# Kernel optimization log

Measured on AMD Instinct MI355X. Metric: run time of the kernel, lower is better.

## Reference

```python
import jax, jax.numpy as jnp
import numpy as np

HID = 128
N_NODES = 50000
N_EDGES = 640000
N_GRAPHS = 64
N_LAYERS = 3
LN_EPS = 1e-5


def _ln(h, g, b):
    mu = jnp.mean(h, axis=-1, keepdims=True)
    v = jnp.mean(jnp.square(h - mu), axis=-1, keepdims=True)
    return (h - mu) * jax.lax.rsqrt(v + LN_EPS) * g + b


def _mlp2(h, W1, b1, g, be, W2, b2):
    # Linear -> ReLU -> LayerNorm -> (Dropout=identity in eval) -> Linear
    h = _ln(jax.nn.relu(h @ W1.T + b1), g, be)
    return h @ W2.T + b2


def _forward(x, edge_index, batch, axis_W1, axis_b1, axis_g, axis_be, axis_W2, axis_b2, org_W1, org_b1, org_g, org_be, org_W2, org_b2, nin_W, nin_b, conv_W1, conv_b1, conv_g, conv_be, conv_W2, conv_b2, eps, ln_g, ln_b, gate_W1, gate_b1, gate_g, gate_be, gate_W2, gate_b2, head_W1, head_b1, head_g, head_be, head_W2, head_b2):
    axis = x[:, 9:12]
    origin = x[:, 12:15]
    others = jnp.concatenate([x[:, :9], x[:, 15:19]], axis=1)  # [N, 13]
    axis_z = _mlp2(axis, axis_W1, axis_b1, axis_g, axis_be, axis_W2, axis_b2)
    org_z = _mlp2(origin, org_W1, org_b1, org_g, org_be, org_W2, org_b2)
    h = jnp.concatenate([others, axis_z, org_z], axis=1) @ nin_W.T + nin_b  # [N, HID]
    src, dst = edge_index[0], edge_index[1]
    n = x.shape[0]
    for l in range(N_LAYERS):
        res = h
        # GIN: sum-aggregate source features into targets (gather + scatter-add)
        agg = jax.ops.segment_sum(h[src], dst, num_segments=n)
        m = (1.0 + eps[l]) * h + agg
        m = _mlp2(m, conv_W1[l], conv_b1[l], conv_g[l], conv_be[l], conv_W2[l], conv_b2[l])
        h = _ln(jax.nn.relu(m), ln_g[l], ln_b[l]) + res
    # AttentionalAggregation: segment softmax over per-graph node gates
    gate = _mlp2(h, gate_W1, gate_b1, gate_g, gate_be, gate_W2, gate_b2)  # [N, 1]
    gmax = jax.ops.segment_max(gate, batch, num_segments=N_GRAPHS)
    e = jnp.exp(gate - gmax[batch])
    denom = jax.ops.segment_sum(e, batch, num_segments=N_GRAPHS)
    attn = e / denom[batch]
    g = jax.ops.segment_sum(attn * h, batch, num_segments=N_GRAPHS)  # [B, HID]
    logit = _mlp2(g, head_W1, head_b1, head_g, head_be, head_W2, head_b2)[:, 0]
    return logit


def setup_inputs() -> dict:
    key = jax.random.key(0)
    ks = iter(jax.random.split(key, 64))
    nk = lambda: next(ks)
    lin = lambda o, i: jax.random.normal(nk(), (o, i), jnp.float32) / np.float32(np.sqrt(i))
    lin3 = lambda L, o, i: jnp.stack([lin(o, i) for _ in range(L)])
    z = lambda *s: jnp.zeros(s, jnp.float32)
    o = lambda *s: jnp.ones(s, jnp.float32)
    inp = {}
    inp['x'] = jax.random.normal(nk(), (N_NODES, 19), jnp.float32)
    inp['edge_index'] = jax.random.randint(nk(), (2, N_EDGES), 0, N_NODES)
    inp['batch'] = jnp.sort(jax.random.randint(nk(), (N_NODES,), 0, N_GRAPHS))
    for p in ('axis', 'org'):
        inp[p + '_W1'] = lin(16, 3); inp[p + '_b1'] = z(16)
        inp[p + '_g'] = o(16); inp[p + '_be'] = z(16)
        inp[p + '_W2'] = lin(16, 16); inp[p + '_b2'] = z(16)
    inp['nin_W'] = lin(HID, 45); inp['nin_b'] = z(HID)
    inp['conv_W1'] = lin3(N_LAYERS, HID, HID); inp['conv_b1'] = z(N_LAYERS, HID)
    inp['conv_g'] = o(N_LAYERS, HID); inp['conv_be'] = z(N_LAYERS, HID)
    inp['conv_W2'] = lin3(N_LAYERS, HID, HID); inp['conv_b2'] = z(N_LAYERS, HID)
    inp['eps'] = z(N_LAYERS)
    inp['ln_g'] = o(N_LAYERS, HID); inp['ln_b'] = z(N_LAYERS, HID)
    for p in ('gate', 'head'):
        inp[p + '_W1'] = lin(HID // 2, HID); inp[p + '_b1'] = z(HID // 2)
        inp[p + '_g'] = o(HID // 2); inp[p + '_be'] = z(HID // 2)
        inp[p + '_W2'] = lin(1, HID // 2); inp[p + '_b2'] = z(1)
    return inp


def reference(x, edge_index, batch, axis_W1, axis_b1, axis_g, axis_be, axis_W2, axis_b2, org_W1, org_b1, org_g, org_be, org_W2, org_b2, nin_W, nin_b, conv_W1, conv_b1, conv_g, conv_be, conv_W2, conv_b2, eps, ln_g, ln_b, gate_W1, gate_b1, gate_g, gate_be, gate_W2, gate_b2, head_W1, head_b1, head_g, head_be, head_W2, head_b2):
    return _forward(x, edge_index, batch, axis_W1, axis_b1, axis_g, axis_be, axis_W2, axis_b2, org_W1, org_b1, org_g, org_be, org_W2, org_b2, nin_W, nin_b, conv_W1, conv_b1, conv_g, conv_be, conv_W2, conv_b2, eps, ln_g, ln_b, gate_W1, gate_b1, gate_g, gate_be, gate_W2, gate_b2, head_W1, head_b1, head_g, head_be, head_W2, head_b2)
```

## Files before the change

kernel.cpp:

```cpp
#include <hip/hip_runtime.h>

#define N_NODESC 50000
#define N_EDGESC 640000
#define N_GRAPHSC 64
#define HIDC 128
#define LN_EPSF 1e-5f
#define POOL_SPLIT 16
#define SCAN_NB 49
#define EGRID ((N_EDGESC + 255) / 256)
#define NGRID_GB ((N_NODESC + 255) / 256)
#define NGRID64 ((N_NODESC + 63) / 64)
#define PREP_ELEMS (8192 + 49152 + 49152)
#define WPREP_NB ((PREP_ELEMS + 255) / 256)

typedef short bf16x8 __attribute__((ext_vector_type(8)));
typedef float f32x4 __attribute__((ext_vector_type(4)));

static __device__ __forceinline__ unsigned ord_enc(float f) {
  unsigned u = __float_as_uint(f);
  return (u & 0x80000000u) ? ~u : (u | 0x80000000u);
}
static __device__ __forceinline__ float ord_dec(unsigned u) {
  return __uint_as_float((u & 0x80000000u) ? (u ^ 0x80000000u) : ~u);
}
static __device__ __forceinline__ unsigned short f2bf(float x) {
  unsigned u = __float_as_uint(x);
  u += 0x7fffu + ((u >> 16) & 1u);
  return (unsigned short)(u >> 16);
}
static __device__ __forceinline__ float bf2f(unsigned short b) {
  return __uint_as_float(((unsigned)b) << 16);
}

static __device__ __forceinline__ void mlp16(float in0, float in1, float in2,
    const float* __restrict__ W1, const float* __restrict__ b1,
    const float* __restrict__ g, const float* __restrict__ be,
    const float* __restrict__ W2, const float* __restrict__ b2,
    float* __restrict__ out) {
  float h[16];
  float s1 = 0.f, s2 = 0.f;
#pragma unroll
  for (int j = 0; j < 16; ++j) {
    float v = b1[j] + W1[j*3+0]*in0 + W1[j*3+1]*in1 + W1[j*3+2]*in2;
    v = fmaxf(v, 0.f);
    h[j] = v; s1 += v; s2 += v*v;
  }
  float mu = s1 * (1.f/16.f);
  float var = fmaxf(s2 * (1.f/16.f) - mu*mu, 0.f);
  float rs = rsqrtf(var + LN_EPSF);
  float z[16];
#pragma unroll
  for (int j = 0; j < 16; ++j) z[j] = (h[j]-mu)*rs*g[j] + be[j];
#pragma unroll
  for (int j = 0; j < 16; ++j) {
    float v = b2[j];
#pragma unroll
    for (int k = 0; k < 16; ++k) v += W2[j*16+k]*z[k];
    out[j] = v;
  }
}

__global__ __launch_bounds__(256) void hist_gbound_kernel(const int* __restrict__ ei,
    int* __restrict__ deg, const int* __restrict__ batch, int* __restrict__ gstart,
    const float* __restrict__ ninW, unsigned short* __restrict__ ninWb,
    const float* __restrict__ cW1, unsigned short* __restrict__ cW1b,
    const float* __restrict__ cW2, unsigned short* __restrict__ cW2b) {
  const int b = blockIdx.x;
  if (b < EGRID) {
    int e = b * 256 + threadIdx.x;
    if (e < N_EDGESC) atomicAdd(&deg[ei[N_EDGESC + e]], 1);
  } else if (b < EGRID + NGRID_GB) {
    int i = (b - EGRID) * 256 + threadIdx.x;
    if (i >= N_NODESC) return;
    int bb = batch[i];
    int prev = (i == 0) ? -1 : batch[i-1];
    for (int g = prev + 1; g <= bb; ++g) gstart[g] = i;
    if (i == N_NODESC - 1) {
      for (int g = bb + 1; g <= N_GRAPHSC; ++g) gstart[g] = N_NODESC;
    }
  } else {
    int i = (b - EGRID - NGRID_GB) * 256 + threadIdx.x;
    if (i < 8192) {
      int f = i >> 6, k = i & 63;
      ninWb[i] = (k < 45) ? f2bf(ninW[f*45 + k]) : (unsigned short)0;
    } else if (i < 8192 + 49152) {
      int j = i - 8192;
      cW1b[j] = f2bf(cW1[j]);
    } else if (i < PREP_ELEMS) {
      int j = i - 8192 - 49152;
      cW2b[j] = f2bf(cW2[j]);
    }
  }
}

__global__ __launch_bounds__(1024) void scan1_kernel(const int* __restrict__ deg,
                                                     int* __restrict__ incl,
                                                     int* __restrict__ bsum) {
  const int b = blockIdx.x, t = threadIdx.x;
  const int i = b * 1024 + t;
  const int lane = t & 63, w = t >> 6;
  int v = (i < N_NODESC) ? deg[i] : 0;
#pragma unroll
  for (int off = 1; off < 64; off <<= 1) {
    int n = __shfl_up(v, off);
    if (lane >= off) v += n;
  }
  __shared__ int wsum[16];
  if (lane == 63) wsum[w] = v;
  __syncthreads();
  if (t == 0) {
    int run = 0;
#pragma unroll
    for (int k = 0; k < 16; ++k) { int x = wsum[k]; wsum[k] = run; run += x; }
  }
  __syncthreads();
  v += wsum[w];
  if (i < N_NODESC) incl[i] = v;
  if (t == 1023) bsum[b] = v;
}

__global__ __launch_bounds__(1024) void scan23_kernel(const int* __restrict__ deg,
                                                      const int* __restrict__ bsum,
                                                      int* __restrict__ rowptr,
                                                      int* __restrict__ cursor) {
  __shared__ int ex[SCAN_NB + 1];
  const int b = blockIdx.x, t = threadIdx.x;
  if (t < 64) {
    int v = (t < SCAN_NB) ? bsum[t] : 0;
    const int orig = v;
#pragma unroll
    for (int off = 1; off < 64; off <<= 1) {
      int n = __shfl_up(v, off);
      if (t >= off) v += n;
    }
    if (t < SCAN_NB) ex[t] = v - orig;
    if (t == SCAN_NB - 1) ex[SCAN_NB] = v;
  }
  __syncthreads();
  const int i = b * 1024 + t;
  if (i < N_NODESC) {
    int excl = rowptr[i] - deg[i] + ex[b];
    rowptr[i] = excl;
    cursor[i] = excl;
  }
  if (b == 0 && t == 0) rowptr[N_NODESC] = ex[SCAN_NB];
}

__global__ __launch_bounds__(256, 4) void scatter_enc_kernel(
    const int* __restrict__ ei, int* __restrict__ cursor, int* __restrict__ esrc,
    const float* __restrict__ x,
    const float* __restrict__ aW1, const float* __restrict__ ab1,
    const float* __restrict__ ag,  const float* __restrict__ abe,
    const float* __restrict__ aW2, const float* __restrict__ ab2,
    const float* __restrict__ oW1, const float* __restrict__ ob1,
    const float* __restrict__ og,  const float* __restrict__ obe,
    const float* __restrict__ oW2, const float* __restrict__ ob2,
    const unsigned short* __restrict__ ninWb, const float* __restrict__ ninb,
    unsigned short* __restrict__ Hb) {
  __shared__ unsigned short Ab[64*136];
  const int t = threadIdx.x;

  if (blockIdx.x >= NGRID64) {
    int e = (blockIdx.x - NGRID64) * 256 + t;
    if (e < N_EDGESC) {
      int d = ei[N_EDGESC + e];
      int slot = atomicAdd(&cursor[d], 1);
      esrc[slot] = ei[e];
    }
    return;
  }

  const int nb = blockIdx.x * 64;

  if (t < 192) {
    const int n = t & 63;
    const int gn = nb + n;
    const int grp = t >> 6;
    if (gn < N_NODESC) {
      const float* xr = x + gn * 19;
      if (grp == 0) {
        float z[16];
        mlp16(xr[9], xr[10], xr[11], aW1, ab1, ag, abe, aW2, ab2, z);
#pragma unroll
        for (int k = 0; k < 16; ++k) Ab[n*136 + 13 + k] = f2bf(z[k]);
      } else if (grp == 1) {
        float z[16];
        mlp16(xr[12], xr[13], xr[14], oW1, ob1, og, obe, oW2, ob2, z);
#pragma unroll
        for (int k = 0; k < 16; ++k) Ab[n*136 + 29 + k] = f2bf(z[k]);
      } else {
#pragma unroll
        for (int k = 0; k < 9; ++k) Ab[n*136 + k] = f2bf(xr[k]);
#pragma unroll
        for (int k = 0; k < 4; ++k) Ab[n*136 + 9 + k] = f2bf(xr[15 + k]);
#pragma unroll
        for (int k = 45; k < 64; ++k) Ab[n*136 + k] = 0;
      }
    } else {
      if (grp == 0) {
#pragma unroll
        for (int k = 0; k < 16; ++k) Ab[n*136 + 13 + k] = 0;
      } else if (grp == 1) {
#pragma unroll
        for (int k = 0; k < 16; ++k) Ab[n*136 + 29 + k] = 0;
      } else {
#pragma unroll
        for (int k = 0; k < 13; ++k) Ab[n*136 + k] = 0;
#pragma unroll
        for (int k = 45; k < 64; ++k) Ab[n*136 + k] = 0;
      }
    }
  }
  __syncthreads();

  const int lane = t & 63, wv = t >> 6;
  const int quad = lane >> 4, l16 = lane & 15;
  const int arow = (wv*16 + l16)*136 + quad*8;
  f32x4 acc[8];
#pragma unroll
  for (int ft = 0; ft < 8; ++ft) acc[ft] = (f32x4){0.f,0.f,0.f,0.f};
#pragma unroll
  for (int ks = 0; ks < 2; ++ks) {
    bf16x8 a = *(const bf16x8*)(const void*)&Ab[arow + ks*32];
#pragma unroll
    for (int ft = 0; ft < 8; ++ft) {
      bf16x8 bfr = *(const bf16x8*)&ninWb[(ft*16 + l16)*64 + quad*8 + ks*32];
      acc[ft] = __builtin_amdgcn_mfma_f32_16x16x32_bf16(a, bfr, acc[ft], 0, 0, 0);
    }
  }
  float bb[8];
#pragma unroll
  for (int ft = 0; ft < 8; ++ft) bb[ft] = ninb[ft*16 + l16];
  __syncthreads();
#pragma unroll
  for (int r = 0; r < 4; ++r) {
    int nloc = wv*16 + quad*4 + r;
#pragma unroll
    for (int ft = 0; ft < 8; ++ft)
      Ab[nloc*136 + ft*16 + l16] = f2bf(acc[ft][r] + bb[ft]);
  }
  __syncthreads();
#pragma unroll
  for (int i = 0; i < 4; ++i) {
    int chunk = t + i*256;
    int n = chunk >> 4, c8 = chunk & 15;
    int gn = nb + n;
    if (gn < N_NODESC)
      *(bf16x8*)&Hb[gn*HIDC + c8*8] = *(const bf16x8*)&Ab[n*136 + c8*8];
  }
}

__global__ __launch_bounds__(128) void agg_kernel(const unsigned short* __restrict__ Hb,
    const int* __restrict__ rowptr, const int* __restrict__ esrc,
    const float* __restrict__ epsp, unsigned short* __restrict__ Mb) {
  const int t = threadIdx.x;
  const int c8 = t & 15;
  const int v  = t >> 4;
  const int node = blockIdx.x * 8 + v;
  if (node >= N_NODESC) return;
  const float e1 = 1.0f + epsp[0];
  bf16x8 h = *(const bf16x8*)&Hb[node*HIDC + c8*8];
  float acc[8];
#pragma unroll
  for (int k = 0; k < 8; ++k) acc[k] = 0.f;
  int s = rowptr[node];
  const int e = rowptr[node+1];
  for (; s + 4 <= e; s += 4) {
    int i0 = esrc[s], i1 = esrc[s+1], i2 = esrc[s+2], i3 = esrc[s+3];
    bf16x8 x0 = *(const bf16x8*)&Hb[i0*HIDC + c8*8];
    bf16x8 x1 = *(const bf16x8*)&Hb[i1*HIDC + c8*8];
    bf16x8 x2 = *(const bf16x8*)&Hb[i2*HIDC + c8*8];
    bf16x8 x3 = *(const bf16x8*)&Hb[i3*HIDC + c8*8];
#pragma unroll
    for (int k = 0; k < 8; ++k)
      acc[k] += (bf2f((unsigned short)x0[k]) + bf2f((unsigned short)x1[k]))
              + (bf2f((unsigned short)x2[k]) + bf2f((unsigned short)x3[k]));
  }
  for (; s < e; ++s) {
    bf16x8 x0 = *(const bf16x8*)&Hb[esrc[s]*HIDC + c8*8];
#pragma unroll
    for (int k = 0; k < 8; ++k) acc[k] += bf2f((unsigned short)x0[k]);
  }
  bf16x8 m8;
#pragma unroll
  for (int k = 0; k < 8; ++k)
    m8[k] = (short)f2bf(e1*bf2f((unsigned short)h[k]) + acc[k]);
  *(bf16x8*)&Mb[node*HIDC + c8*8] = m8;
}

template<bool GATE>
__global__ __launch_bounds__(256, 3) void gemmpair_kernel(
    const unsigned short* __restrict__ Mb,
    const unsigned short* __restrict__ Hin,
    const unsigned short* __restrict__ W1b, const float* __restrict__ b1,
    const float* __restrict__ g1, const float* __restrict__ be1,
    const unsigned short* __restrict__ W2b, const float* __restrict__ b2,
    const float* __restrict__ lng, const float* __restrict__ lnb,
    unsigned short* __restrict__ Hout,
    const float* __restrict__ gW1, const float* __restrict__ gb1,
    const float* __restrict__ glng, const float* __restrict__ glnb,
    const float* __restrict__ gW2, const float* __restrict__ gb2,
    const int* __restrict__ batch, float* __restrict__ gateb,
    unsigned* __restrict__ gmaxu) {
  __shared__ unsigned short Ab[64*136];
  __shared__ unsigned short Wl[128*136];
  __shared__ unsigned sgm[N_GRAPHSC];
  const int t = threadIdx.x;
  const int nb = blockIdx.x * 64;
  if (GATE && t < N_GRAPHSC) sgm[t] = 0u;

#pragma unroll
  for (int i = 0; i < 4; ++i) {
    int chunk = t + i*256;
    int n = chunk >> 4, c8 = chunk & 15;
    int gn = nb + n;
    bf16x8 v = {0,0,0,0,0,0,0,0};
    if (gn < N_NODESC) v = *(const bf16x8*)&Mb[gn*HIDC + c8*8];
    *(bf16x8*)&Ab[n*136 + c8*8] = v;
  }
#pragma unroll
  for (int i = 0; i < 8; ++i) {
    int q = t + i*256;
    int f = q >> 4, c8 = q & 15;
    *(bf16x8*)&Wl[f*136 + c8*8] = *(const bf16x8*)&W1b[f*HIDC + c8*8];
  }
  __syncthreads();

  const int lane = t & 63, wv = t >> 6;
  const int quad = lane >> 4, l16 = lane & 15;
  const int arow = (wv*16 + l16)*136 + quad*8;

  f32x4 acc[8];
#pragma unroll
  for (int ft = 0; ft < 8; ++ft) acc[ft] = (f32x4){0.f,0.f,0.f,0.f};
#pragma unroll
  for (int ks = 0; ks < 4; ++ks) {
    bf16x8 a = *(const bf16x8*)(const void*)&Ab[arow + ks*32];
#pragma unroll
    for (int ft = 0; ft < 8; ++ft) {
      bf16x8 b = *(const bf16x8*)(const void*)&Wl[(ft*16 + l16)*136 + quad*8 + ks*32];
      acc[ft] = __builtin_amdgcn_mfma_f32_16x16x32_bf16(a, b, acc[ft], 0, 0, 0);
    }
  }

  {
    float bb[8], gg[8], bee[8];
#pragma unroll
    for (int ft = 0; ft < 8; ++ft) {
      int f = ft*16 + l16;
      bb[ft] = b1[f]; gg[ft] = g1[f]; bee[ft] = be1[f];
    }
    float s1[4] = {0,0,0,0}, s2[4] = {0,0,0,0};
#pragma unroll
    for (int ft = 0; ft < 8; ++ft)
#pragma unroll
      for (int r = 0; r < 4; ++r) {
        float v = fmaxf(acc[ft][r] + bb[ft], 0.f);
        acc[ft][r] = v; s1[r] += v; s2[r] += v*v;
      }
#pragma unroll
    for (int m = 1; m < 16; m <<= 1)
#pragma unroll
      for (int r = 0; r < 4; ++r) {
        s1[r] += __shfl_xor(s1[r], m);
        s2[r] += __shfl_xor(s2[r], m);
      }
    float mu[4], rs[4];
#pragma unroll
    for (int r = 0; r < 4; ++r) {
      mu[r] = s1[r] * (1.f/128.f);
      float var = fmaxf(s2[r] * (1.f/128.f) - mu[r]*mu[r], 0.f);
      rs[r] = rsqrtf(var + LN_EPSF);
    }
    __syncthreads();
#pragma unroll
    for (int r = 0; r < 4; ++r) {
      int nloc = wv*16 + quad*4 + r;
#pragma unroll
      for (int ft = 0; ft < 8; ++ft) {
        float o = (acc[ft][r] - mu[r])*rs[r]*gg[ft] + bee[ft];
        Ab[nloc*136 + ft*16 + l16] = f2bf(o);
      }
    }
  }
#pragma unroll
  for (int i = 0; i < 8; ++i) {
    int q = t + i*256;
    int f = q >> 4, c8 = q & 15;
    *(bf16x8*)&Wl[f*136 + c8*8] = *(const bf16x8*)&W2b[f*HIDC + c8*8];
  }
  __syncthreads();

#pragma unroll
  for (int ft = 0; ft < 8; ++ft) acc[ft] = (f32x4){0.f,0.f,0.f,0.f};
#pragma unroll
  for (int ks = 0; ks < 4; ++ks) {
    bf16x8 a = *(const bf16x8*)(const void*)&Ab[arow + ks*32];
#pragma unroll
    for (int ft = 0; ft < 8; ++ft) {
      bf16x8 b = *(const bf16x8*)(const void*)&Wl[(ft*16 + l16)*136 + quad*8 + ks*32];
      acc[ft] = __builtin_amdgcn_mfma_f32_16x16x32_bf16(a, b, acc[ft], 0, 0, 0);
    }
  }

  {
    float bb[8], gg[8], bee[8];
#pragma unroll
    for (int ft = 0; ft < 8; ++ft) {
      int f = ft*16 + l16;
      bb[ft] = b2[f]; gg[ft] = lng[f]; bee[ft] = lnb[f];
    }
    float s1[4] = {0,0,0,0}, s2[4] = {0,0,0,0};
#pragma unroll
    for (int ft = 0; ft < 8; ++ft)
#pragma unroll
      for (int r = 0; r < 4; ++r) {
        float v = fmaxf(acc[ft][r] + bb[ft], 0.f);
        acc[ft][r] = v; s1[r] += v; s2[r] += v*v;
      }
#pragma unroll
    for (int m = 1; m < 16; m <<= 1)
#pragma unroll
      for (int r = 0; r < 4; ++r) {
        s1[r] += __shfl_xor(s1[r], m);
        s2[r] += __shfl_xor(s2[r], m);
      }
    float mu[4], rs[4];
#pragma unroll
    for (int r = 0; r < 4; ++r) {
      mu[r] = s1[r] * (1.f/128.f);
      float var = fmaxf(s2[r] * (1.f/128.f) - mu[r]*mu[r], 0.f);
      rs[r] = rsqrtf(var + LN_EPSF);
    }
    __syncthreads();
#pragma unroll
    for (int r = 0; r < 4; ++r) {
      int nloc = wv*16 + quad*4 + r;
#pragma unroll
      for (int ft = 0; ft < 8; ++ft) {
        float o = (acc[ft][r] - mu[r])*rs[r]*gg[ft] + bee[ft];
        Ab[nloc*136 + ft*16 + l16] = f2bf(o);
      }
    }
  }
  __syncthreads();
#pragma unroll
  for (int i = 0; i < 4; ++i) {
    int chunk = t + i*256;
    int n = chunk >> 4, cc = chunk & 15;
    int gn = nb + n;
    bf16x8 o8 = {0,0,0,0,0,0,0,0};
    if (gn < N_NODESC) {
      bf16x8 vv = *(const bf16x8*)&Ab[n*136 + cc*8];
      bf16x8 rr = *(const bf16x8*)&Hin[gn*HIDC + cc*8];
#pragma unroll
      for (int k = 0; k < 8; ++k)
        o8[k] = (short)f2bf(bf2f((unsigned short)vv[k]) + bf2f((unsigned short)rr[k]));
      *(bf16x8*)&Hout[gn*HIDC + cc*8] = o8;
    }
    if (GATE) *(bf16x8*)&Ab[n*136 + cc*8] = o8;
  }

  if (GATE) {
#pragma unroll
    for (int i = 0; i < 8; ++i) {
      int q = t + i*256;
      int f = q >> 5, c4 = q & 31;
      float4 v = *(const float4*)&gW1[f*HIDC + c4*4];
      ushort4 hh;
      hh.x = f2bf(v.x); hh.y = f2bf(v.y); hh.z = f2bf(v.z); hh.w = f2bf(v.w);
      *(ushort4*)&Wl[f*136 + c4*4] = hh;
    }
    __syncthreads();

    f32x4 gacc[4];
#pragma unroll
    for (int ft = 0; ft < 4; ++ft) gacc[ft] = (f32x4){0.f,0.f,0.f,0.f};
#pragma unroll
    for (int ks = 0; ks < 4; ++ks) {
      bf16x8 a = *(const bf16x8*)(const void*)&Ab[arow + ks*32];
#pragma unroll
      for (int ft = 0; ft < 4; ++ft) {
        bf16x8 b = *(const bf16x8*)(const void*)&Wl[(ft*16 + l16)*136 + quad*8 + ks*32];
        gacc[ft] = __builtin_amdgcn_mfma_f32_16x16x32_bf16(a, b, gacc[ft], 0, 0, 0);
      }
    }

    float bb[4], gg[4], bee[4], w2v[4];
#pragma unroll
    for (int ft = 0; ft < 4; ++ft) {
      int f = ft*16 + l16;
      bb[ft] = gb1[f]; gg[ft] = glng[f]; bee[ft] = glnb[f]; w2v[ft] = gW2[f];
    }
    float s1[4] = {0,0,0,0}, s2[4] = {0,0,0,0};
#pragma unroll
    for (int ft = 0; ft < 4; ++ft)
#pragma unroll
      for (int r = 0; r < 4; ++r) {
        float v = fmaxf(gacc[ft][r] + bb[ft], 0.f);
        gacc[ft][r] = v; s1[r] += v; s2[r] += v*v;
      }
#pragma unroll
    for (int m = 1; m < 16; m <<= 1)
#pragma unroll
      for (int r = 0; r < 4; ++r) {
        s1[r] += __shfl_xor(s1[r], m);
        s2[r] += __shfl_xor(s2[r], m);
      }
    float pd[4];
#pragma unroll
    for (int r = 0; r < 4; ++r) {
      float mu = s1[r] * (1.f/64.f);
      float var = fmaxf(s2[r] * (1.f/64.f) - mu*mu, 0.f);
      float rs = rsqrtf(var + LN_EPSF);
      float p = 0.f;
#pragma unroll
      for (int ft = 0; ft < 4; ++ft)
        p += ((gacc[ft][r] - mu)*rs*gg[ft] + bee[ft]) * w2v[ft];
      pd[r] = p;
    }
#pragma unroll
    for (int m = 1; m < 16; m <<= 1)
#pragma unroll
      for (int r = 0; r < 4; ++r) pd[r] += __shfl_xor(pd[r], m);
    if (l16 == 0) {
      float b2v = gb2[0];
#pragma unroll
      for (int r = 0; r < 4; ++r) {
        int node = nb + wv*16 + quad*4 + r;
        if (node < N_NODESC) {
          float gv = pd[r] + b2v;
          gateb[node] = gv;
          atomicMax(&sgm[batch[node]], ord_enc(gv));
        }
      }
    }
    __syncthreads();
    if (t < N_GRAPHSC && sgm[t] != 0u) atomicMax(&gmaxu[t], sgm[t]);
  }
}

__global__ __launch_bounds__(256) void pool_kernel(const unsigned short* __restrict__ Hb,
    const float* __restrict__ gateb, const int* __restrict__ gstart,
    const unsigned* __restrict__ gmaxu, float* __restrict__ S,
    float* __restrict__ denom) {
  const int g    = blockIdx.x / POOL_SPLIT;
  const int part = blockIdx.x % POOL_SPLIT;
  const int s0 = gstart[g], s1 = gstart[g+1];
  const int cnt = s1 - s0;
  const int chunk = (cnt + POOL_SPLIT - 1) / POOL_SPLIT;
  int lo = s0 + part * chunk;
  int hi = lo + chunk; if (hi > s1) hi = s1;
  const int t = threadIdx.x;
  const int c8 = t & 15;
  const int v  = t >> 4;
  const float gm = ord_dec(gmaxu[g]);
  float acc[8];
#pragma unroll
  for (int k = 0; k < 8; ++k) acc[k] = 0.f;
  float de = 0.f;
  for (int n = lo + v; n < hi; n += 16) {
    float e = expf(gateb[n] - gm);
    bf16x8 hv = *(const bf16x8*)&Hb[n*HIDC + c8*8];
#pragma unroll
    for (int k = 0; k < 8; ++k) acc[k] += e * bf2f((unsigned short)hv[k]);
    if (c8 == 0) de += e;
  }
  __shared__ float sacc[16*128];
  __shared__ float sden[16];
#pragma unroll
  for (int k = 0; k < 8; ++k) sacc[v*128 + c8*8 + k] = acc[k];
  if (c8 == 0) sden[v] = de;
  __syncthreads();
  if (t < 128) {
    float s = 0.f;
#pragma unroll
    for (int vv = 0; vv < 16; ++vv) s += sacc[vv*128 + t];
    atomicAdd(&S[g*HIDC + t], s);
  }
  if (t == 0) {
    float d = 0.f;
#pragma unroll
    for (int vv = 0; vv < 16; ++vv) d += sden[vv];
    atomicAdd(&denom[g], d);
  }
}

__global__ __launch_bounds__(64) void head_kernel(const float* __restrict__ S,
    const float* __restrict__ denom, const float* __restrict__ W1,
    const float* __restrict__ b1, const float* __restrict__ g,
    const float* __restrict__ be, const float* __restrict__ W2,
    const float* __restrict__ b2, float* __restrict__ out) {
  const int gr = blockIdx.x;
  const int j = threadIdx.x;
  const float inv = 1.0f / denom[gr];
  float v = b1[j];
  for (int k = 0; k < HIDC; ++k) v += (S[gr*HIDC + k] * inv) * W1[j*HIDC + k];
  v = fmaxf(v, 0.f);
  float s1 = v, s2 = v*v;
  for (int off = 32; off; off >>= 1) { s1 += __shfl_xor(s1, off); s2 += __shfl_xor(s2, off); }
  float mu = s1 * (1.f/64.f);
  float var = fmaxf(s2 * (1.f/64.f) - mu*mu, 0.f);
  float rs = rsqrtf(var + LN_EPSF);
  float z = (v-mu)*rs*g[j] + be[j];
  float p = z * W2[j];
  for (int off = 32; off; off >>= 1) p += __shfl_xor(p, off);
  if (j == 0) out[gr] = p + b2[0];
}

extern "C" void kernel_launch(void* const* d_in, const int* in_sizes, int n_in,
                              void* d_out, int out_size, void* d_ws, size_t ws_size,
                              hipStream_t stream) {
  (void)in_sizes; (void)n_in; (void)out_size; (void)ws_size;
  const float* x     = (const float*)d_in[0];
  const int*   ei    = (const int*)d_in[1];
  const int*   batch = (const int*)d_in[2];
  const float* aW1 = (const float*)d_in[3];
  const float* ab1 = (const float*)d_in[4];
  const float* ag  = (const float*)d_in[5];
  const float* abe = (const float*)d_in[6];
  const float* aW2 = (const float*)d_in[7];
  const float* ab2 = (const float*)d_in[8];
  const float* oW1 = (const float*)d_in[9];
  const float* ob1 = (const float*)d_in[10];
  const float* og  = (const float*)d_in[11];
  const float* obe = (const float*)d_in[12];
  const float* oW2 = (const float*)d_in[13];
  const float* ob2 = (const float*)d_in[14];
  const float* ninW = (const float*)d_in[15];
  const float* ninb = (const float*)d_in[16];
  const float* cW1 = (const float*)d_in[17];
  const float* cb1 = (const float*)d_in[18];
  const float* cg  = (const float*)d_in[19];
  const float* cbe = (const float*)d_in[20];
  const float* cW2 = (const float*)d_in[21];
  const float* cb2 = (const float*)d_in[22];
  const float* eps = (const float*)d_in[23];
  const float* lng = (const float*)d_in[24];
  const float* lnb = (const float*)d_in[25];
  const float* gW1 = (const float*)d_in[26];
  const float* gb1 = (const float*)d_in[27];
  const float* gg  = (const float*)d_in[28];
  const float* gbe = (const float*)d_in[29];
  const float* gW2 = (const float*)d_in[30];
  const float* gb2 = (const float*)d_in[31];
  const float* hW1 = (const float*)d_in[32];
  const float* hb1 = (const float*)d_in[33];
  const float* hg  = (const float*)d_in[34];
  const float* hbe = (const float*)d_in[35];
  const float* hW2 = (const float*)d_in[36];
  const float* hb2 = (const float*)d_in[37];

  char* ws = (char*)d_ws;
  unsigned short* Ha = (unsigned short*)(ws + 0);
  unsigned short* Hc = (unsigned short*)(ws + 12800000);
  unsigned short* Mb = (unsigned short*)(ws + 25600000);
  float* gateb = (float*)(ws + 38400000);
  int*   deg   = (int*)(ws + 38600000);
  float* S     = (float*)(ws + 38800000);
  float* denom = (float*)(ws + 38832768);
  unsigned* gmaxu = (unsigned*)(ws + 38833024);
  int* rowptr  = (int*)(ws + 38833280);
  int* cursor  = (int*)(ws + 39033284);
  int* esrc    = (int*)(ws + 39233284);
  int* bsum    = (int*)(ws + 41793284);
  int* gstart  = (int*)(ws + 41793540);
  unsigned short* ninWb = (unsigned short*)(ws + 41800000);
  unsigned short* cW1b  = (unsigned short*)(ws + 41816384);
  unsigned short* cW2b  = (unsigned short*)(ws + 41914688);

  hipMemsetAsync(deg, 0, 233280, stream);

  hist_gbound_kernel<<<EGRID + NGRID_GB + WPREP_NB, 256, 0, stream>>>(
      ei, deg, batch, gstart, ninW, ninWb, cW1, cW1b, cW2, cW2b);
  scan1_kernel<<<SCAN_NB, 1024, 0, stream>>>(deg, rowptr, bsum);
  scan23_kernel<<<SCAN_NB, 1024, 0, stream>>>(deg, bsum, rowptr, cursor);
  scatter_enc_kernel<<<NGRID64 + EGRID, 256, 0, stream>>>(
      ei, cursor, esrc,
      x, aW1, ab1, ag, abe, aW2, ab2,
      oW1, ob1, og, obe, oW2, ob2,
      ninWb, ninb, Ha);

  unsigned short* cur = Ha;
  unsigned short* nxt = Hc;
  for (int l = 0; l < 3; ++l) {
    agg_kernel<<<(N_NODESC + 7) / 8, 128, 0, stream>>>(cur, rowptr, esrc, eps + l, Mb);
    if (l < 2) {
      gemmpair_kernel<false><<<NGRID64, 256, 0, stream>>>(
          Mb, cur,
          cW1b + l*HIDC*HIDC, cb1 + l*HIDC, cg + l*HIDC, cbe + l*HIDC,
          cW2b + l*HIDC*HIDC, cb2 + l*HIDC, lng + l*HIDC, lnb + l*HIDC,
          nxt,
          gW1, gb1, gg, gbe, gW2, gb2, batch, gateb, gmaxu);
    } else {
      gemmpair_kernel<true><<<NGRID64, 256, 0, stream>>>(
          Mb, cur,
          cW1b + l*HIDC*HIDC, cb1 + l*HIDC, cg + l*HIDC, cbe + l*HIDC,
          cW2b + l*HIDC*HIDC, cb2 + l*HIDC, lng + l*HIDC, lnb + l*HIDC,
          nxt,
          gW1, gb1, gg, gbe, gW2, gb2, batch, gateb, gmaxu);
    }
    unsigned short* tmp = cur; cur = nxt; nxt = tmp;
  }

  pool_kernel<<<N_GRAPHSC * POOL_SPLIT, 256, 0, stream>>>(Hc, gateb, gstart, gmaxu, S, denom);
  head_kernel<<<N_GRAPHSC, 64, 0, stream>>>(S, denom, hW1, hb1, hg, hbe, hW2, hb2,
                                            (float*)d_out);
}
```

Before: 373.3 us.

## Pad degree/cursor counters to separate cache lines and unroll aggregation by eight

Degree and cursor atomic counters are spread out with a 32-int stride (128 B) so concurrent atomics on neighbouring nodes no longer share cache lines. They live in the Mb buffer region, which is free during preprocessing. The edge-scatter blocks are placed at the front of the combined grid so atomics get scheduled ahead of the encoder work. The aggregation loop adds an 8-way unrolled gather for more memory-level parallelism. In exchange it memsets 6.4 MB instead of about 233 KB, and the strided reads in the scan kernels are uncoalesced.

```diff
diff --git a/kernel.cpp b/kernel.cpp
--- a/kernel.cpp
+++ b/kernel.cpp
@@ -12,6 +12,7 @@
 #define NGRID64 ((N_NODESC + 63) / 64)
 #define PREP_ELEMS (8192 + 49152 + 49152)
 #define WPREP_NB ((PREP_ELEMS + 255) / 256)
+#define CSTR 32
 
 typedef short bf16x8 __attribute__((ext_vector_type(8)));
 typedef float f32x4 __attribute__((ext_vector_type(4)));
@@ -61,14 +62,14 @@
 }
 
 __global__ __launch_bounds__(256) void hist_gbound_kernel(const int* __restrict__ ei,
-    int* __restrict__ deg, const int* __restrict__ batch, int* __restrict__ gstart,
+    int* __restrict__ deg_p, const int* __restrict__ batch, int* __restrict__ gstart,
     const float* __restrict__ ninW, unsigned short* __restrict__ ninWb,
     const float* __restrict__ cW1, unsigned short* __restrict__ cW1b,
     const float* __restrict__ cW2, unsigned short* __restrict__ cW2b) {
   const int b = blockIdx.x;
   if (b < EGRID) {
     int e = b * 256 + threadIdx.x;
-    if (e < N_EDGESC) atomicAdd(&deg[ei[N_EDGESC + e]], 1);
+    if (e < N_EDGESC) atomicAdd(&deg_p[ei[N_EDGESC + e] * CSTR], 1);
   } else if (b < EGRID + NGRID_GB) {
     int i = (b - EGRID) * 256 + threadIdx.x;
     if (i >= N_NODESC) return;
@@ -93,13 +94,13 @@
   }
 }
 
-__global__ __launch_bounds__(1024) void scan1_kernel(const int* __restrict__ deg,
+__global__ __launch_bounds__(1024) void scan1_kernel(const int* __restrict__ deg_p,
                                                      int* __restrict__ incl,
                                                      int* __restrict__ bsum) {
   const int b = blockIdx.x, t = threadIdx.x;
   const int i = b * 1024 + t;
   const int lane = t & 63, w = t >> 6;
-  int v = (i < N_NODESC) ? deg[i] : 0;
+  int v = (i < N_NODESC) ? deg_p[i * CSTR] : 0;
 #pragma unroll
   for (int off = 1; off < 64; off <<= 1) {
     int n = __shfl_up(v, off);
@@ -119,10 +120,10 @@
   if (t == 1023) bsum[b] = v;
 }
 
-__global__ __launch_bounds__(1024) void scan23_kernel(const int* __restrict__ deg,
+__global__ __launch_bounds__(1024) void scan23_kernel(const int* __restrict__ deg_p,
                                                       const int* __restrict__ bsum,
                                                       int* __restrict__ rowptr,
-                                                      int* __restrict__ cursor) {
+                                                      int* __restrict__ cursor_p) {
   __shared__ int ex[SCAN_NB + 1];
   const int b = blockIdx.x, t = threadIdx.x;
   if (t < 64) {
@@ -139,15 +140,15 @@
   __syncthreads();
   const int i = b * 1024 + t;
   if (i < N_NODESC) {
-    int excl = rowptr[i] - deg[i] + ex[b];
+    int excl = rowptr[i] - deg_p[i * CSTR] + ex[b];
     rowptr[i] = excl;
-    cursor[i] = excl;
+    cursor_p[i * CSTR] = excl;
   }
   if (b == 0 && t == 0) rowptr[N_NODESC] = ex[SCAN_NB];
 }
 
 __global__ __launch_bounds__(256, 4) void scatter_enc_kernel(
-    const int* __restrict__ ei, int* __restrict__ cursor, int* __restrict__ esrc,
+    const int* __restrict__ ei, int* __restrict__ cursor_p, int* __restrict__ esrc,
     const float* __restrict__ x,
     const float* __restrict__ aW1, const float* __restrict__ ab1,
     const float* __restrict__ ag,  const float* __restrict__ abe,
@@ -160,17 +161,17 @@
   __shared__ unsigned short Ab[64*136];
   const int t = threadIdx.x;
 
-  if (blockIdx.x >= NGRID64) {
-    int e = (blockIdx.x - NGRID64) * 256 + t;
+  if (blockIdx.x < EGRID) {
+    int e = blockIdx.x * 256 + t;
     if (e < N_EDGESC) {
       int d = ei[N_EDGESC + e];
-      int slot = atomicAdd(&cursor[d], 1);
+      int slot = atomicAdd(&cursor_p[d * CSTR], 1);
       esrc[slot] = ei[e];
     }
     return;
   }
 
-  const int nb = blockIdx.x * 64;
+  const int nb = (blockIdx.x - EGRID) * 64;
 
   if (t < 192) {
     const int n = t & 63;
@@ -265,6 +266,24 @@
   for (int k = 0; k < 8; ++k) acc[k] = 0.f;
   int s = rowptr[node];
   const int e = rowptr[node+1];
+  for (; s + 8 <= e; s += 8) {
+    int i0 = esrc[s],   i1 = esrc[s+1], i2 = esrc[s+2], i3 = esrc[s+3];
+    int i4 = esrc[s+4], i5 = esrc[s+5], i6 = esrc[s+6], i7 = esrc[s+7];
+    bf16x8 x0 = *(const bf16x8*)&Hb[i0*HIDC + c8*8];
+    bf16x8 x1 = *(const bf16x8*)&Hb[i1*HIDC + c8*8];
+    bf16x8 x2 = *(const bf16x8*)&Hb[i2*HIDC + c8*8];
+    bf16x8 x3 = *(const bf16x8*)&Hb[i3*HIDC + c8*8];
+    bf16x8 x4 = *(const bf16x8*)&Hb[i4*HIDC + c8*8];
+    bf16x8 x5 = *(const bf16x8*)&Hb[i5*HIDC + c8*8];
+    bf16x8 x6 = *(const bf16x8*)&Hb[i6*HIDC + c8*8];
+    bf16x8 x7 = *(const bf16x8*)&Hb[i7*HIDC + c8*8];
+#pragma unroll
+    for (int k = 0; k < 8; ++k)
+      acc[k] += ((bf2f((unsigned short)x0[k]) + bf2f((unsigned short)x1[k]))
+               + (bf2f((unsigned short)x2[k]) + bf2f((unsigned short)x3[k])))
+              + ((bf2f((unsigned short)x4[k]) + bf2f((unsigned short)x5[k]))
+               + (bf2f((unsigned short)x6[k]) + bf2f((unsigned short)x7[k])));
+  }
   for (; s + 4 <= e; s += 4) {
     int i0 = esrc[s], i1 = esrc[s+1], i2 = esrc[s+2], i3 = esrc[s+3];
     bf16x8 x0 = *(const bf16x8*)&Hb[i0*HIDC + c8*8];
@@ -655,13 +674,13 @@
   unsigned short* Ha = (unsigned short*)(ws + 0);
   unsigned short* Hc = (unsigned short*)(ws + 12800000);
   unsigned short* Mb = (unsigned short*)(ws + 25600000);
+  int* deg_p    = (int*)(ws + 25600000);
+  int* cursor_p = (int*)(ws + 32000000);
   float* gateb = (float*)(ws + 38400000);
-  int*   deg   = (int*)(ws + 38600000);
   float* S     = (float*)(ws + 38800000);
   float* denom = (float*)(ws + 38832768);
   unsigned* gmaxu = (unsigned*)(ws + 38833024);
   int* rowptr  = (int*)(ws + 38833280);
-  int* cursor  = (int*)(ws + 39033284);
   int* esrc    = (int*)(ws + 39233284);
   int* bsum    = (int*)(ws + 41793284);
   int* gstart  = (int*)(ws + 41793540);
@@ -669,14 +688,15 @@
   unsigned short* cW1b  = (unsigned short*)(ws + 41816384);
   unsigned short* cW2b  = (unsigned short*)(ws + 41914688);
 
-  hipMemsetAsync(deg, 0, 233280, stream);
+  hipMemsetAsync(deg_p, 0, 6400000, stream);
+  hipMemsetAsync(S, 0, 33280, stream);
 
   hist_gbound_kernel<<<EGRID + NGRID_GB + WPREP_NB, 256, 0, stream>>>(
-      ei, deg, batch, gstart, ninW, ninWb, cW1, cW1b, cW2, cW2b);
-  scan1_kernel<<<SCAN_NB, 1024, 0, stream>>>(deg, rowptr, bsum);
-  scan23_kernel<<<SCAN_NB, 1024, 0, stream>>>(deg, bsum, rowptr, cursor);
-  scatter_enc_kernel<<<NGRID64 + EGRID, 256, 0, stream>>>(
-      ei, cursor, esrc,
+      ei, deg_p, batch, gstart, ninW, ninWb, cW1, cW1b, cW2, cW2b);
+  scan1_kernel<<<SCAN_NB, 1024, 0, stream>>>(deg_p, rowptr, bsum);
+  scan23_kernel<<<SCAN_NB, 1024, 0, stream>>>(deg_p, bsum, rowptr, cursor_p);
+  scatter_enc_kernel<<<EGRID + NGRID64, 256, 0, stream>>>(
+      ei, cursor_p, esrc,
       x, aW1, ab1, ag, abe, aW2, ab2,
       oW1, ob1, og, obe, oW2, ob2,
       ninWb, ninb, Ha);
```

After: 363.1 us. 1.03x faster.
